# Optimization experiments

Hardware: AMD Instinct MI355X
Metric: run time of the kernel (lower is better)

Reference implementation:

```python
import jax, jax.numpy as jnp
import numpy as np

N_NODES = 20000
N_EDGES = 640000
D = 128


def setup_inputs() -> dict:
    key = jax.random.key(0)
    ks = jax.random.split(key, 8)
    scale = 1.0 / np.sqrt(D)
    x = jax.random.normal(ks[0], (N_NODES, D), dtype=jnp.float32)
    edge_index = jax.random.randint(ks[1], (2, N_EDGES), 0, N_NODES, dtype=jnp.int64)
    W1_rel = jax.random.normal(ks[2], (D, D), dtype=jnp.float32) * scale
    b1_rel = jnp.zeros((D,), dtype=jnp.float32)
    W1_root = jax.random.normal(ks[3], (D, D), dtype=jnp.float32) * scale
    W2_rel = jax.random.normal(ks[4], (D, D), dtype=jnp.float32) * scale
    b2_rel = jnp.zeros((D,), dtype=jnp.float32)
    W2_root = jax.random.normal(ks[5], (D, D), dtype=jnp.float32) * scale
    return {"x": x, "edge_index": edge_index,
            "W1_rel": W1_rel, "b1_rel": b1_rel, "W1_root": W1_root,
            "W2_rel": W2_rel, "b2_rel": b2_rel, "W2_root": W2_root}


def _graph_conv(x, src, dst, W_rel, b_rel, W_root):
    # sum-aggregate neighbor features: gather from src, scatter-add to dst
    agg = jax.ops.segment_sum(x[src], dst, num_segments=N_NODES)  # [N, D]
    # PyG GraphConv: lin_rel(agg) (with bias) + lin_root(x) (no bias)
    return agg @ W_rel + b_rel + x @ W_root


def reference(x, edge_index, W1_rel, b1_rel, W1_root, W2_rel, b2_rel, W2_root):
    src, dst = edge_index[0], edge_index[1]  # messages flow src (j) -> dst (i)
    h = jax.nn.relu(_graph_conv(x, src, dst, W1_rel, b1_rel, W1_root))
    out = _graph_conv(h, src, dst, W2_rel, b2_rel, W2_root)  # final ReLU stripped
    return out
```

## Files before the change

kernel.cpp:

```cpp
#include <hip/hip_runtime.h>

#define N_NODES 20000
#define N_EDGES 640000
#define D 128
#define CAP 128

typedef __attribute__((ext_vector_type(8))) short bf16x8;
typedef __attribute__((ext_vector_type(4))) float f32x4;

__device__ __forceinline__ short f2bf(float f) {
    union { float f; unsigned u; } un; un.f = f;
    unsigned r = un.u + 0x7fff + ((un.u >> 16) & 1);
    return (short)(r >> 16);
}
__device__ __forceinline__ float bflo(unsigned u) { return __uint_as_float(u << 16); }
__device__ __forceinline__ float bfhi(unsigned u) { return __uint_as_float(u & 0xffff0000u); }

__global__ __launch_bounds__(256) void prep_kernel(
    const float* __restrict__ x,
    const int* __restrict__ src, const int* __restrict__ dst,
    const float* __restrict__ W1_rel, const float* __restrict__ W1_root,
    const float* __restrict__ W2_rel, const float* __restrict__ W2_root,
    int* __restrict__ cnt, unsigned short* __restrict__ buckets,
    short* __restrict__ xb, short* __restrict__ wpk1, short* __restrict__ wpk2)
{
    const int b = blockIdx.x;
    const int tid = threadIdx.x;
    if (b < 625) {
        int e4 = b * 256 + tid;
        int4 s4 = ((const int4*)src)[e4];
        int4 d4 = ((const int4*)dst)[e4];
#pragma unroll
        for (int q = 0; q < 4; q++) {
            int d = (&d4.x)[q];
            int s = (&s4.x)[q];
            int p = atomicAdd(&cnt[d], 1);
            if (p < CAP) buckets[(d << 7) + p] = (unsigned short)s;
        }
    } else if (b < 3125) {
        int i = (b - 625) * 256 + tid;
        float4 v = ((const float4*)x)[i];
        ushort4 o;
        o.x = (unsigned short)f2bf(v.x);
        o.y = (unsigned short)f2bf(v.y);
        o.z = (unsigned short)f2bf(v.z);
        o.w = (unsigned short)f2bf(v.w);
        ((ushort4*)xb)[i] = o;
    } else {
        int pb  = b - 3125;
        int job = pb >> 4;
        int idx = (pb & 15) * 256 + tid;
        const float* Wrel  = job ? W2_rel  : W1_rel;
        const float* Wroot = job ? W2_root : W1_root;
        short* Wpk = job ? wpk2 : wpk1;
        int lane = idx & 63;
        int ct   = (idx >> 6) & 7;
        int t    = idx >> 9;
        const float* W = (t < 4) ? Wrel : Wroot;
        int k0  = (t & 3) * 32 + (lane >> 4) * 8;
        int col = ct * 16 + (lane & 15);
        bf16x8 pk;
#pragma unroll
        for (int j = 0; j < 8; j++)
            pk[j] = f2bf(W[(size_t)(k0 + j) * D + col]);
        ((bf16x8*)Wpk)[idx] = pk;
    }
}

template <bool RELU, bool OUT_BF16>
__global__ __launch_bounds__(512) void layer_kernel(
    const short* __restrict__ xin,
    const int* __restrict__ cnt,
    const unsigned short* __restrict__ buckets,
    const short* __restrict__ Wpk,
    const float* __restrict__ brel,
    void* __restrict__ outp)
{
    __shared__ short sAgg[16][136];
    __shared__ int nextNode;

    const int tid  = threadIdx.x;
    const int row0 = blockIdx.x * 16;
    const int lane = tid & 63;

    if (tid == 0) nextNode = 0;
    __syncthreads();

    for (;;) {
        int pos = 0;
        if (lane == 0) pos = atomicAdd(&nextNode, 1);
        pos = __shfl(pos, 0, 64);
        if (pos >= 16) break;

        const int node = row0 + pos;
        int n = cnt[node];
        n = (n > CAP) ? CAP : n;
        unsigned idxw = *(const unsigned*)(buckets + (node << 7) + lane * 2);
        const short* xbase = xin + lane * 2;

        float acx = 0.f, acy = 0.f;
        int i = 0;
        for (; i + 8 <= n; i += 8) {
            unsigned u[8];
#pragma unroll
            for (int q = 0; q < 8; q++) {
                int j = i + q;
                unsigned w = __shfl(idxw, j >> 1, 64);
                unsigned sidx = (j & 1) ? (w >> 16) : (w & 0xffffu);
                u[q] = *(const unsigned*)(xbase + (size_t)sidx * D);
            }
#pragma unroll
            for (int q = 0; q < 8; q++) { acx += bflo(u[q]); acy += bfhi(u[q]); }
        }
        for (; i < n; i++) {
            unsigned w = __shfl(idxw, i >> 1, 64);
            unsigned sidx = (i & 1) ? (w >> 16) : (w & 0xffffu);
            unsigned u0 = *(const unsigned*)(xbase + (size_t)sidx * D);
            acx += bflo(u0); acy += bfhi(u0);
        }
        unsigned pk = ((unsigned)(unsigned short)f2bf(acx))
                    | (((unsigned)(unsigned short)f2bf(acy)) << 16);
        *(unsigned*)&sAgg[pos][lane * 2] = pk;
    }
    __syncthreads();

    const int wave = tid >> 6;
    const int quad = lane >> 4;
    const int l16  = lane & 15;

    f32x4 acc = (f32x4){0.f, 0.f, 0.f, 0.f};
    const short* arow_x = xin + (size_t)(row0 + l16) * D + quad * 8;
    const bf16x8* wb = (const bf16x8*)Wpk + lane;

#pragma unroll
    for (int t = 0; t < 8; t++) {
        bf16x8 a;
        if (t < 4)
            a = *(const bf16x8*)&sAgg[l16][(t & 3) * 32 + quad * 8];
        else
            a = *(const bf16x8*)(arow_x + (t & 3) * 32);
        bf16x8 bfr = wb[(t * 8 + wave) * 64];
        acc = __builtin_amdgcn_mfma_f32_16x16x32_bf16(a, bfr, acc, 0, 0, 0);
    }

    const int col  = wave * 16 + l16;
    const int orow = row0 + quad * 4;
    const float bias = brel[col];
#pragma unroll
    for (int r = 0; r < 4; r++) {
        float v = acc[r] + bias;
        if (RELU) v = fmaxf(v, 0.f);
        if (OUT_BF16)
            ((short*)outp)[(size_t)(orow + r) * D + col] = f2bf(v);
        else
            ((float*)outp)[(size_t)(orow + r) * D + col] = v;
    }
}

extern "C" void kernel_launch(void* const* d_in, const int* in_sizes, int n_in,
                              void* d_out, int out_size, void* d_ws, size_t ws_size,
                              hipStream_t stream) {
    const float* x       = (const float*)d_in[0];
    const int*   ei      = (const int*)  d_in[1];
    const float* W1_rel  = (const float*)d_in[2];
    const float* b1_rel  = (const float*)d_in[3];
    const float* W1_root = (const float*)d_in[4];
    const float* W2_rel  = (const float*)d_in[5];
    const float* b2_rel  = (const float*)d_in[6];
    const float* W2_root = (const float*)d_in[7];
    float* out = (float*)d_out;

    char* p = (char*)d_ws;
    short* xb   = (short*)p;  p += (size_t)N_NODES * D * 2;
    short* hb   = (short*)p;  p += (size_t)N_NODES * D * 2;
    short* wpk1 = (short*)p;  p += 65536;
    short* wpk2 = (short*)p;  p += 65536;
    int*   cnt  = (int*)p;    p += (size_t)N_NODES * 4;
    unsigned short* buckets = (unsigned short*)p;

    const int* src = ei;
    const int* dst = ei + N_EDGES;

    const int layerblocks = N_NODES / 16;

    hipMemsetAsync(cnt, 0, (size_t)N_NODES * sizeof(int), stream);
    prep_kernel<<<3157, 256, 0, stream>>>(
        x, src, dst, W1_rel, W1_root, W2_rel, W2_root,
        cnt, buckets, xb, wpk1, wpk2);

    layer_kernel<true, true><<<layerblocks, 512, 0, stream>>>(
        xb, cnt, buckets, wpk1, b1_rel, (void*)hb);

    layer_kernel<false, false><<<layerblocks, 512, 0, stream>>>(
        hb, cnt, buckets, wpk2, b2_rel, (void*)out);
}
```

Baseline: 174.8 us.

## Gather four neighbors per wave with 16-byte loads and static node assignment

Each wave now owns two fixed nodes instead of pulling node positions from a shared atomic counter. Within a wave, four 16-lane groups each fetch a different neighbor row using 16-byte loads, with 8 bf16 values per lane. Partial sums are then combined across the groups with xor shuffles. Bucket indices are read as scalar-uniform uint2 words rather than shuffled per edge. This raises memory-level parallelism and cuts shuffle and atomic overhead, at the cost of more registers and some wasted lanes when degree is not a multiple of four or exceeds 64.

```diff
diff --git a/kernel.cpp b/kernel.cpp
--- a/kernel.cpp
+++ b/kernel.cpp
@@ -15,6 +15,9 @@
 }
 __device__ __forceinline__ float bflo(unsigned u) { return __uint_as_float(u << 16); }
 __device__ __forceinline__ float bfhi(unsigned u) { return __uint_as_float(u & 0xffff0000u); }
+__device__ __forceinline__ unsigned pk2(float a, float b) {
+    return ((unsigned)(unsigned short)f2bf(a)) | (((unsigned)(unsigned short)f2bf(b)) << 16);
+}
 
 __global__ __launch_bounds__(256) void prep_kernel(
     const float* __restrict__ x,
@@ -77,57 +80,72 @@
     void* __restrict__ outp)
 {
     __shared__ short sAgg[16][136];
-    __shared__ int nextNode;
 
     const int tid  = threadIdx.x;
     const int row0 = blockIdx.x * 16;
     const int lane = tid & 63;
-
-    if (tid == 0) nextNode = 0;
-    __syncthreads();
-
-    for (;;) {
-        int pos = 0;
-        if (lane == 0) pos = atomicAdd(&nextNode, 1);
-        pos = __shfl(pos, 0, 64);
-        if (pos >= 16) break;
-
-        const int node = row0 + pos;
+    const int wv   = tid >> 6;
+    const int q    = lane >> 4;
+    const int l16  = lane & 15;
+
+    for (int rep = 0; rep < 2; rep++) {
+        const int pos  = wv * 2 + rep;
+        const int node = __builtin_amdgcn_readfirstlane(row0 + pos);
         int n = cnt[node];
         n = (n > CAP) ? CAP : n;
-        unsigned idxw = *(const unsigned*)(buckets + (node << 7) + lane * 2);
-        const short* xbase = xin + lane * 2;
-
-        float acx = 0.f, acy = 0.f;
-        int i = 0;
-        for (; i + 8 <= n; i += 8) {
-            unsigned u[8];
-#pragma unroll
-            for (int q = 0; q < 8; q++) {
-                int j = i + q;
-                unsigned w = __shfl(idxw, j >> 1, 64);
-                unsigned sidx = (j & 1) ? (w >> 16) : (w & 0xffffu);
-                u[q] = *(const unsigned*)(xbase + (size_t)sidx * D);
+        n = __builtin_amdgcn_readfirstlane(n);
+        const unsigned short* br = buckets + ((size_t)node << 7);
+
+        uint2 w[16];
+#pragma unroll
+        for (int g = 0; g < 16; g++)
+            w[g] = *(const uint2*)(br + g * 4);
+
+        float acc[8] = {0.f, 0.f, 0.f, 0.f, 0.f, 0.f, 0.f, 0.f};
+        const short* xbase = xin + l16 * 8;
+
+#pragma unroll
+        for (int g = 0; g < 16; g++) {
+            if (g * 4 < n) {
+                unsigned wsel = (q & 2) ? w[g].y : w[g].x;
+                unsigned sidx = (wsel >> ((q & 1) * 16)) & 0xffffu;
+                uint4 v = *(const uint4*)(xbase + (size_t)sidx * D);
+                if (g * 4 + q < n) {
+                    acc[0] += bflo(v.x); acc[1] += bfhi(v.x);
+                    acc[2] += bflo(v.y); acc[3] += bfhi(v.y);
+                    acc[4] += bflo(v.z); acc[5] += bfhi(v.z);
+                    acc[6] += bflo(v.w); acc[7] += bfhi(v.w);
+                }
             }
-#pragma unroll
-            for (int q = 0; q < 8; q++) { acx += bflo(u[q]); acy += bfhi(u[q]); }
-        }
-        for (; i < n; i++) {
-            unsigned w = __shfl(idxw, i >> 1, 64);
-            unsigned sidx = (i & 1) ? (w >> 16) : (w & 0xffffu);
-            unsigned u0 = *(const unsigned*)(xbase + (size_t)sidx * D);
-            acx += bflo(u0); acy += bfhi(u0);
-        }
-        unsigned pk = ((unsigned)(unsigned short)f2bf(acx))
-                    | (((unsigned)(unsigned short)f2bf(acy)) << 16);
-        *(unsigned*)&sAgg[pos][lane * 2] = pk;
+        }
+        for (int i = 64; i < n; i++) {
+            unsigned sidx = br[i];
+            uint4 v = *(const uint4*)(xbase + (size_t)sidx * D);
+            if (q == 0) {
+                acc[0] += bflo(v.x); acc[1] += bfhi(v.x);
+                acc[2] += bflo(v.y); acc[3] += bfhi(v.y);
+                acc[4] += bflo(v.z); acc[5] += bfhi(v.z);
+                acc[6] += bflo(v.w); acc[7] += bfhi(v.w);
+            }
+        }
+
+#pragma unroll
+        for (int c = 0; c < 8; c++) {
+            acc[c] += __shfl_xor(acc[c], 16, 64);
+            acc[c] += __shfl_xor(acc[c], 32, 64);
+        }
+        if (q == 0) {
+            uint4 o;
+            o.x = pk2(acc[0], acc[1]);
+            o.y = pk2(acc[2], acc[3]);
+            o.z = pk2(acc[4], acc[5]);
+            o.w = pk2(acc[6], acc[7]);
+            *(uint4*)&sAgg[pos][l16 * 8] = o;
+        }
     }
     __syncthreads();
 
-    const int wave = tid >> 6;
     const int quad = lane >> 4;
-    const int l16  = lane & 15;
-
     f32x4 acc = (f32x4){0.f, 0.f, 0.f, 0.f};
     const short* arow_x = xin + (size_t)(row0 + l16) * D + quad * 8;
     const bf16x8* wb = (const bf16x8*)Wpk + lane;
@@ -139,11 +157,11 @@
             a = *(const bf16x8*)&sAgg[l16][(t & 3) * 32 + quad * 8];
         else
             a = *(const bf16x8*)(arow_x + (t & 3) * 32);
-        bf16x8 bfr = wb[(t * 8 + wave) * 64];
+        bf16x8 bfr = wb[(t * 8 + wv) * 64];
         acc = __builtin_amdgcn_mfma_f32_16x16x32_bf16(a, bfr, acc, 0, 0, 0);
     }
 
-    const int col  = wave * 16 + l16;
+    const int col  = wv * 16 + l16;
     const int orow = row0 + quad * 4;
     const float bias = brel[col];
 #pragma unroll
```

Measured after the change: 243.4 us. 39.2% more time.
